# Kernel optimization log

Measured on AMD Instinct MI355X. Metric: run time of the kernel, lower is better.

## Reference

```python
import jax, jax.numpy as jnp
import numpy as np
import math

NUM_GRIDS = 128
INPUT_DIM = 128
OUTPUT_DIM = 128
BATCH = 8192
INIT_SCALE = 0.1


def _borders_cdf_grid(n_chunks):
    # inverse Laplace CDF grid borders, exactly as in the torch module
    def inv(u):
        return np.log(2.0 * u) if u <= 0.5 else -np.log(2.0 * (1.0 - u))
    cs = 1.0 / n_chunks
    b = [inv(i * cs) for i in range(1, n_chunks)]
    left = b[0] - (b[1] - b[0])
    right = b[-1] + (b[-1] - b[-2])
    return np.array([left] + b + [right], dtype=np.float32)  # [n_chunks+1]


def setup_inputs() -> dict:
    key = jax.random.key(0)
    kx, kp = jax.random.split(key)
    x = jax.random.normal(kx, (INPUT_DIM, BATCH), dtype=jnp.float32)
    s = INIT_SCALE / math.sqrt(INPUT_DIM)
    func_parameter = jax.random.uniform(
        kp, (NUM_GRIDS + 1, OUTPUT_DIM, INPUT_DIM), dtype=jnp.float32,
        minval=-s, maxval=s)
    borders = jnp.asarray(_borders_cdf_grid(NUM_GRIDS))
    inverse_chunk_lengths = 1.0 / (borders[1:] - borders[:-1])  # [NUM_GRIDS]
    return {"x": x, "func_parameter": func_parameter,
            "borders": borders, "inverse_chunk_lengths": inverse_chunk_lengths}


def reference(x, func_parameter, borders, inverse_chunk_lengths):
    # x: [I, B]; func_parameter: [G+1, O, I]
    G = borders.shape[0] - 1
    I = x.shape[0]
    # Laplace CDF: R -> [0, 1]
    exp_na = jnp.exp(-jnp.abs(x))
    cdf = jnp.where(x > 0, 1.0 - 0.5 * exp_na, 0.5 * exp_na)
    # bucketize on uniform CDF grid (truncation == floor since cdf*G >= 0)
    idx = jnp.clip((cdf * G).astype(jnp.int32), 0, G - 1)        # [I, B]
    idx_next = jnp.clip(idx + 1, 0, G)                           # [I, B]
    left = borders[idx]                                          # [I, B]
    inv_len = inverse_chunk_lengths[idx]                         # [I, B]
    d = (x - left) * inv_len                                     # [I, B]
    # gather per-input-dim parameter rows: val[i, b, o] = P[idx[i,b], o, i]
    Pt = jnp.transpose(func_parameter, (2, 0, 1))                # [I, G+1, O]
    rows = jnp.arange(I)[:, None]                                # [I, 1]
    val_l = Pt[rows, idx]                                        # [I, B, O]
    val_r = Pt[rows, idx_next]                                   # [I, B, O]
    out = ((1.0 - d)[..., None] * val_l + d[..., None] * val_r).sum(axis=0)  # [B, O]
    return out.T                                                 # [O, B]
```

## Files before the change

### kernel.cpp

```cpp
#include <hip/hip_runtime.h>
#include <cstdint>


#define NG 128
#define NI 128
#define NO 128
#define NB 8192
#define WO 4
#define PH 8
#define NPH (NI / PH)

using half2v = __attribute__((ext_vector_type(2))) _Float16;

__device__ inline uint32_t pack_f16x2(float lo, float hi) {
    _Float16 hl = (_Float16)lo, hh = (_Float16)hi;
    return (uint32_t)__builtin_bit_cast(unsigned short, hl) |
           ((uint32_t)__builtin_bit_cast(unsigned short, hh) << 16);
}

__global__ __launch_bounds__(256) void build_q(const float* __restrict__ P,
                                               uint32_t* __restrict__ Q2) {
    __shared__ float lp[32][129];
    __shared__ float ln[32][129];
    const int g  = blockIdx.x >> 2;
    const int o0 = (blockIdx.x & 3) * 32;
    const int t  = threadIdx.x;
    #pragma unroll
    for (int p = 0; p < 16; ++p) {
        int e = p * 256 + t;
        int ol = e >> 7, i = e & 127;
        lp[ol][i] = P[(size_t)(g * NO + o0 + ol) * NI + i];
        ln[ol][i] = P[(size_t)((g + 1) * NO + o0 + ol) * NI + i];
    }
    __syncthreads();
    #pragma unroll
    for (int p = 0; p < 4; ++p) {
        int e = p * 256 + t;
        int sl = e >> 7, i = e & 127;
        uint32_t r[4];
        #pragma unroll
        for (int ow = 0; ow < 4; ++ow) {
            float pl = lp[sl * 4 + ow][i];
            float dd = ln[sl * 4 + ow][i] - pl;
            r[ow] = pack_f16x2(pl, dd);
        }
        int s = (o0 >> 2) + sl;
        *(uint4*)(Q2 + ((size_t)(s * NI + i) * NG + g) * 4) =
            make_uint4(r[0], r[1], r[2], r[3]);
    }
}

__global__ __launch_bounds__(256) void build_t(const float* __restrict__ x,
                                               const float* __restrict__ borders,
                                               const float* __restrict__ icl,
                                               uint32_t* __restrict__ T) {
    const int e0 = (blockIdx.x * 256 + threadIdx.x) * 4;
    const float4 xv = *(const float4*)(x + e0);
    uint32_t r[4];
    const float xs[4] = {xv.x, xv.y, xv.z, xv.w};
    #pragma unroll
    for (int k = 0; k < 4; ++k) {
        float v = xs[k];
        float ea = __expf(-fabsf(v));
        float cdf = v > 0.f ? 1.f - 0.5f * ea : 0.5f * ea;
        int idx = (int)(cdf * 128.f);
        idx = idx > 127 ? 127 : idx;
        float d = (v - borders[idx]) * icl[idx];
        _Float16 hd = (_Float16)d;
        r[k] = (uint32_t)idx |
               ((uint32_t)__builtin_bit_cast(unsigned short, hd) << 16);
    }
    *(uint4*)(T + e0) = make_uint4(r[0], r[1], r[2], r[3]);
}

__global__ __launch_bounds__(1024) void main_k(const uint32_t* __restrict__ Q2,
                                               const uint32_t* __restrict__ T,
                                               float* __restrict__ out) {
    __shared__ uint32_t slab[2][PH][NG * WO];
    const int t    = threadIdx.x;
    const int wv   = t >> 6;
    const int lane = t & 63;
    const int bx   = blockIdx.x;
    const int s    = bx & 31;
    const int bblk = (bx >> 5) << 10;
    const int bme  = bblk + (wv << 6) + lane;
    const uint32_t* Qs = Q2 + (size_t)s * NI * NG * WO;
    const int st_il = wv >> 1;
    const int st_k  = ((wv & 1) << 8) + (lane << 2);

    float a0 = 0.f, a1 = 0.f, a2 = 0.f, a3 = 0.f;

    {
        const uint32_t* src = Qs + (size_t)st_il * (NG * WO) + st_k;
        __builtin_amdgcn_global_load_lds(
            (const __attribute__((address_space(1))) uint32_t*)src,
            (__attribute__((address_space(3))) uint32_t*)&slab[0][st_il][st_k],
            16, 0, 0);
    }
    __syncthreads();

    for (int p = 0; p < NPH; ++p) {
        const int cur = p & 1;
        if (p < NPH - 1) {
            const uint32_t* src =
                Qs + (size_t)((p + 1) * PH + st_il) * (NG * WO) + st_k;
            __builtin_amdgcn_global_load_lds(
                (const __attribute__((address_space(1))) uint32_t*)src,
                (__attribute__((address_space(3))) uint32_t*)
                    &slab[cur ^ 1][st_il][st_k],
                16, 0, 0);
        }
        const uint32_t* Trow = T + (size_t)p * PH * NB + bme;
        #pragma unroll
        for (int il = 0; il < PH; ++il) {
            uint32_t tw  = Trow[(size_t)il * NB];
            uint32_t w2b = (tw & 0xFFFF0000u) | 0x3C00u;
            uint32_t off = (tw & 127u) << 2;
            uint4 q = *(const uint4*)&slab[cur][il][off];
            half2v w2 = __builtin_bit_cast(half2v, w2b);
            a0 = __builtin_amdgcn_fdot2(__builtin_bit_cast(half2v, q.x), w2, a0, false);
            a1 = __builtin_amdgcn_fdot2(__builtin_bit_cast(half2v, q.y), w2, a1, false);
            a2 = __builtin_amdgcn_fdot2(__builtin_bit_cast(half2v, q.z), w2, a2, false);
            a3 = __builtin_amdgcn_fdot2(__builtin_bit_cast(half2v, q.w), w2, a3, false);
        }
        __syncthreads();
    }

    size_t ob = (size_t)(s * 4) * NB + bme;
    __builtin_nontemporal_store(a0, out + ob);
    __builtin_nontemporal_store(a1, out + ob + NB);
    __builtin_nontemporal_store(a2, out + ob + 2 * (size_t)NB);
    __builtin_nontemporal_store(a3, out + ob + 3 * (size_t)NB);
}

extern "C" void kernel_launch(void* const* d_in, const int* in_sizes, int n_in,
                              void* d_out, int out_size, void* d_ws, size_t ws_size,
                              hipStream_t stream) {
    const float* x       = (const float*)d_in[0];
    const float* P       = (const float*)d_in[1];
    const float* borders = (const float*)d_in[2];
    const float* icl     = (const float*)d_in[3];
    float* out = (float*)d_out;

    uint32_t* Q2 = (uint32_t*)d_ws;
    uint32_t* T  = Q2 + (size_t)NO * NI * NG;

    hipLaunchKernelGGL(build_q, dim3(NG * 4), dim3(256), 0, stream, P, Q2);
    hipLaunchKernelGGL(build_t, dim3(NI * NB / 1024), dim3(256), 0, stream,
                       x, borders, icl, T);
    hipLaunchKernelGGL(main_k, dim3((NB / 1024) * 32), dim3(1024), 0, stream,
                       Q2, T, out);
}
```

Measured before the change: 101.0 us.

## Register-prefetch Q slab and T words a phase ahead, prescale index offsets

The main kernel now loads the next phase's Q slab into registers with ordinary global loads and writes it to LDS after the current compute, replacing the async global_load_lds path. The T words for the next phase are also prefetched into registers, and the loop is fully unrolled. build_t stores the index pre-shifted into a byte offset, which removes a shift and mask per lookup. The change is meant to hide global latency behind the fdot2 work, at the cost of higher register pressure at 1024 threads per block and an extra register-to-LDS store.

```diff
diff --git a/kernel.cpp b/kernel.cpp
--- a/kernel.cpp
+++ b/kernel.cpp
@@ -67,7 +67,7 @@
         idx = idx > 127 ? 127 : idx;
         float d = (v - borders[idx]) * icl[idx];
         _Float16 hd = (_Float16)d;
-        r[k] = (uint32_t)idx |
+        r[k] = ((uint32_t)idx << 4) |
                ((uint32_t)__builtin_bit_cast(unsigned short, hd) << 16);
     }
     *(uint4*)(T + e0) = make_uint4(r[0], r[1], r[2], r[3]);
@@ -78,52 +78,55 @@
                                                float* __restrict__ out) {
     __shared__ uint32_t slab[2][PH][NG * WO];
     const int t    = threadIdx.x;
-    const int wv   = t >> 6;
-    const int lane = t & 63;
     const int bx   = blockIdx.x;
     const int s    = bx & 31;
     const int bblk = (bx >> 5) << 10;
-    const int bme  = bblk + (wv << 6) + lane;
+    const int bme  = bblk + t;
     const uint32_t* Qs = Q2 + (size_t)s * NI * NG * WO;
-    const int st_il = wv >> 1;
-    const int st_k  = ((wv & 1) << 8) + (lane << 2);
 
     float a0 = 0.f, a1 = 0.f, a2 = 0.f, a3 = 0.f;
 
+    uint32_t treg[PH];
     {
-        const uint32_t* src = Qs + (size_t)st_il * (NG * WO) + st_k;
-        __builtin_amdgcn_global_load_lds(
-            (const __attribute__((address_space(1))) uint32_t*)src,
-            (__attribute__((address_space(3))) uint32_t*)&slab[0][st_il][st_k],
-            16, 0, 0);
+        uint4 q0 = *(const uint4*)(Qs + (size_t)t * 4);
+        #pragma unroll
+        for (int il = 0; il < PH; ++il)
+            treg[il] = T[(size_t)il * NB + bme];
+        ((uint4*)&slab[0][0][0])[t] = q0;
     }
     __syncthreads();
 
+    #pragma unroll
     for (int p = 0; p < NPH; ++p) {
         const int cur = p & 1;
+        uint32_t tnxt[PH];
+        uint4 qnxt;
         if (p < NPH - 1) {
-            const uint32_t* src =
-                Qs + (size_t)((p + 1) * PH + st_il) * (NG * WO) + st_k;
-            __builtin_amdgcn_global_load_lds(
-                (const __attribute__((address_space(1))) uint32_t*)src,
-                (__attribute__((address_space(3))) uint32_t*)
-                    &slab[cur ^ 1][st_il][st_k],
-                16, 0, 0);
+            qnxt = *(const uint4*)(Qs + (size_t)(p + 1) * (PH * NG * WO) +
+                                   (size_t)t * 4);
+            #pragma unroll
+            for (int il = 0; il < PH; ++il)
+                tnxt[il] = T[(size_t)((p + 1) * PH + il) * NB + bme];
         }
-        const uint32_t* Trow = T + (size_t)p * PH * NB + bme;
         #pragma unroll
         for (int il = 0; il < PH; ++il) {
-            uint32_t tw  = Trow[(size_t)il * NB];
+            uint32_t tw  = treg[il];
+            uint32_t off = tw & 0xFFFFu;
             uint32_t w2b = (tw & 0xFFFF0000u) | 0x3C00u;
-            uint32_t off = (tw & 127u) << 2;
-            uint4 q = *(const uint4*)&slab[cur][il][off];
+            uint4 q = *(const uint4*)((const char*)&slab[cur][il][0] + off);
             half2v w2 = __builtin_bit_cast(half2v, w2b);
             a0 = __builtin_amdgcn_fdot2(__builtin_bit_cast(half2v, q.x), w2, a0, false);
             a1 = __builtin_amdgcn_fdot2(__builtin_bit_cast(half2v, q.y), w2, a1, false);
             a2 = __builtin_amdgcn_fdot2(__builtin_bit_cast(half2v, q.z), w2, a2, false);
             a3 = __builtin_amdgcn_fdot2(__builtin_bit_cast(half2v, q.w), w2, a3, false);
         }
-        __syncthreads();
+        if (p < NPH - 1) {
+            ((uint4*)&slab[cur ^ 1][0][0])[t] = qnxt;
+            #pragma unroll
+            for (int il = 0; il < PH; ++il)
+                treg[il] = tnxt[il];
+            __syncthreads();
+        }
     }
 
     size_t ob = (size_t)(s * 4) * NB + bme;
```

Result: faster. 93.72 us (-7.2%).
